# Performance work log

Measured on AMD Instinct MI355X. Metric: run time of the kernel, lower is better.

The kernel has to match this reference:

```python
import jax, jax.numpy as jnp
import numpy as np

DIM = 1024
HEADS = 16
DIM_HEAD = 64
INNER = HEADS * DIM_HEAD
EPS = 1e-6


def elu_feature_map(t):
    # F.elu(x) + 1
    return jnp.where(t > 0, t + 1.0, jnp.exp(t))


def setup_inputs() -> dict:
    key = jax.random.key(0)
    k1, k2, k3, k4 = jax.random.split(key, 4)
    B, N = 4, 8192
    x = jax.random.normal(k1, (B, N, DIM), dtype=jnp.float32)
    s_in = 1.0 / np.sqrt(DIM)
    s_out = 1.0 / np.sqrt(INNER)
    Wqkv = jax.random.uniform(k2, (DIM, 3 * INNER), dtype=jnp.float32, minval=-s_in, maxval=s_in)
    Wout = jax.random.uniform(k3, (INNER, DIM), dtype=jnp.float32, minval=-s_out, maxval=s_out)
    bout = jax.random.uniform(k4, (DIM,), dtype=jnp.float32, minval=-s_out, maxval=s_out)
    return {"x": x, "Wqkv": Wqkv, "Wout": Wout, "bout": bout}


def reference(x, Wqkv, Wout, bout):
    B, N, D = x.shape
    qkv = x @ Wqkv  # [B,N,3*INNER]
    q, k, v = jnp.split(qkv, 3, axis=-1)
    # b n (h d) -> b h n d
    resh = lambda t: t.reshape(B, N, HEADS, DIM_HEAD).transpose(0, 2, 1, 3)
    q, k, v = resh(q), resh(k), resh(v)
    q = elu_feature_map(q)
    k = elu_feature_map(k)
    kv = jnp.einsum('bhnd,bhnf->bhdf', k, v)          # [B,H,d,d]
    k_sum = k.sum(axis=-2)                             # [B,H,d]
    qkv_out = jnp.einsum('bhnd,bhdf->bhnf', q, kv)    # [B,H,N,d]
    q_k_sum = jnp.einsum('bhnd,bhd->bhn', q, k_sum)   # [B,H,N]
    out = qkv_out / (q_k_sum[..., None] + EPS)
    out = out.transpose(0, 2, 1, 3).reshape(B, N, INNER)  # b h n d -> b n (h d)
    return out @ Wout + bout
```

## Files before the change

### kernel.cpp

```cpp
#include <hip/hip_runtime.h>
#include <hip/hip_bf16.h>
#include <math.h>


typedef unsigned short ushort_t;
typedef __attribute__((ext_vector_type(8))) short s8v;
typedef __attribute__((ext_vector_type(4))) float f32x4;

#define MFMA(a,b,c) __builtin_amdgcn_mfma_f32_16x16x32_bf16((a),(b),(c),0,0,0)

typedef __attribute__((address_space(3))) unsigned int as3_u32;
typedef __attribute__((address_space(1))) const unsigned int as1_u32c;

__device__ __forceinline__ void g2l16(const void* g, void* l) {
    __builtin_amdgcn_global_load_lds((as1_u32c*)g, (as3_u32*)l, 16, 0, 0);
}

__device__ __forceinline__ float bf2f(ushort_t u) {
    union { float f; unsigned v; } x; x.v = ((unsigned)u) << 16; return x.f;
}
__device__ __forceinline__ ushort_t f2bf(float f) {
    union { float f; unsigned v; } x; x.f = f;
    unsigned r = x.v + 0x7fffu + ((x.v >> 16) & 1u);
    return (ushort_t)(r >> 16);
}
__device__ __forceinline__ float elu1(float t) { return t > 0.0f ? t + 1.0f : expf(t); }

__global__ void k_cast(const float* __restrict__ in, ushort_t* __restrict__ out, int n8) {
    int i = blockIdx.x * blockDim.x + threadIdx.x;
    if (i >= n8) return;
    const float4* p = (const float4*)in;
    float4 a = p[(size_t)i * 2], b = p[(size_t)i * 2 + 1];
    uint4 o;
    o.x = (unsigned)f2bf(a.x) | ((unsigned)f2bf(a.y) << 16);
    o.y = (unsigned)f2bf(a.z) | ((unsigned)f2bf(a.w) << 16);
    o.z = (unsigned)f2bf(b.x) | ((unsigned)f2bf(b.y) << 16);
    o.w = (unsigned)f2bf(b.z) | ((unsigned)f2bf(b.w) << 16);
    *(uint4*)(out + (size_t)i * 8) = o;
}

__global__ __launch_bounds__(256) void k_transpose(const float* __restrict__ W,
                                                   ushort_t* __restrict__ WT, int K, int N) {
    __shared__ float s[32][33];
    const int t = threadIdx.x;
    const int k0 = blockIdx.x * 32, n0 = blockIdx.y * 32;
    const int kr = t >> 3, n4 = (t & 7) * 4;
    float4 v = *(const float4*)(W + (size_t)(k0 + kr) * N + n0 + n4);
    s[kr][n4 + 0] = v.x; s[kr][n4 + 1] = v.y; s[kr][n4 + 2] = v.z; s[kr][n4 + 3] = v.w;
    __syncthreads();
    const int nr = kr, k4 = n4;
    unsigned lo = (unsigned)f2bf(s[k4 + 0][nr]) | ((unsigned)f2bf(s[k4 + 1][nr]) << 16);
    unsigned hi = (unsigned)f2bf(s[k4 + 2][nr]) | ((unsigned)f2bf(s[k4 + 3][nr]) << 16);
    *(uint2*)(WT + (size_t)(n0 + nr) * K + k0 + k4) = make_uint2(lo, hi);
}

template<int MODE>
__global__ __launch_bounds__(512, 2) void k_gemm(
    const ushort_t* __restrict__ A, const ushort_t* __restrict__ B,
    ushort_t* __restrict__ obf, const float* __restrict__ bout, float* __restrict__ of)
{
    constexpr int ASZ  = 256 * 64;
    constexpr int BUFS = 2 * ASZ;
    constexpr int NBN  = (MODE == 0) ? 12 : 4;
    constexpr int CH   = (128 * NBN) / 8;
    __shared__ ushort_t lds[2 * BUFS];

    const int t = threadIdx.x, l = t & 63, w = t >> 6;
    const int wr = w >> 2, wc = w & 3;
    const int orig = blockIdx.x;
    const int wg   = (orig & 7) * CH + (orig >> 3);
    const size_t m0 = (size_t)(wg / NBN) * 256;
    const size_t n0 = (size_t)(wg % NBN) * 256;

    f32x4 acc[8][4];
    const f32x4 z = {0.f, 0.f, 0.f, 0.f};
#pragma unroll
    for (int i = 0; i < 8; i++)
#pragma unroll
        for (int j = 0; j < 4; j++) acc[i][j] = z;

    const int lr  = l >> 3;
    const int lco = ((l & 7) ^ lr) << 3;
    const ushort_t* gA = A + (m0 + (size_t)(32 * w) + lr) * 1024 + lco;
    const ushort_t* gB = B + (n0 + (size_t)(32 * w) + lr) * 1024 + lco;
    const int la15 = l & 15;
    const int exo  = (((l >> 4) ^ (l & 7)) << 3);

#pragma unroll
    for (int i = 0; i < 4; i++)
        g2l16(gA + (size_t)(8 * i) * 1024, &lds[(w * 4 + i) * 512]);
#pragma unroll
    for (int i = 0; i < 4; i++)
        g2l16(gB + (size_t)(8 * i) * 1024, &lds[ASZ + (w * 4 + i) * 512]);
    asm volatile("s_waitcnt vmcnt(0)" ::: "memory");
    __builtin_amdgcn_sched_barrier(0);
    __builtin_amdgcn_s_barrier();
    __builtin_amdgcn_sched_barrier(0);

    for (int T = 0; T < 16; ++T) {
        const int base  = (T & 1) * BUFS;
        const int nbase = BUFS - base;

        if (T < 15) {
            const size_t k1 = (size_t)(T + 1) * 64;
#pragma unroll
            for (int i = 0; i < 4; i++)
                g2l16(gA + (size_t)(8 * i) * 1024 + k1, &lds[nbase + (w * 4 + i) * 512]);
#pragma unroll
            for (int i = 0; i < 4; i++)
                g2l16(gB + (size_t)(8 * i) * 1024 + k1, &lds[nbase + ASZ + (w * 4 + i) * 512]);
        }

        s8v af[8], bf[4];
#pragma unroll
        for (int nf = 0; nf < 4; nf++)
            bf[nf] = *(const s8v*)&lds[base + ASZ + (wc * 64 + nf * 16 + la15) * 64 + exo];
#pragma unroll
        for (int mf = 0; mf < 8; mf++)
            af[mf] = *(const s8v*)&lds[base + (wr * 128 + mf * 16 + la15) * 64 + exo];
        __builtin_amdgcn_s_setprio(1);
#pragma unroll
        for (int mf = 0; mf < 8; mf++)
#pragma unroll
            for (int nf = 0; nf < 4; nf++)
                acc[mf][nf] = MFMA(af[mf], bf[nf], acc[mf][nf]);
        __builtin_amdgcn_s_setprio(0);
#pragma unroll
        for (int nf = 0; nf < 4; nf++)
            bf[nf] = *(const s8v*)&lds[base + ASZ + (wc * 64 + nf * 16 + la15) * 64 + (32 ^ exo)];
#pragma unroll
        for (int mf = 0; mf < 8; mf++)
            af[mf] = *(const s8v*)&lds[base + (wr * 128 + mf * 16 + la15) * 64 + (32 ^ exo)];
        __builtin_amdgcn_s_setprio(1);
#pragma unroll
        for (int mf = 0; mf < 8; mf++)
#pragma unroll
            for (int nf = 0; nf < 4; nf++)
                acc[mf][nf] = MFMA(af[mf], bf[nf], acc[mf][nf]);
        __builtin_amdgcn_s_setprio(0);

        if (T < 15) {
            __builtin_amdgcn_sched_barrier(0);
            asm volatile("s_waitcnt vmcnt(0)" ::: "memory");
            __builtin_amdgcn_sched_barrier(0);
            __builtin_amdgcn_s_barrier();
            __builtin_amdgcn_sched_barrier(0);
        }
    }

    const int r4 = (l >> 4) * 4;
    if (MODE == 0) {
#pragma unroll
        for (int mf = 0; mf < 8; mf++)
#pragma unroll
            for (int nf = 0; nf < 4; nf++) {
                const size_t colb = n0 + wc * 64 + nf * 16;
                const bool feat = colb < 2048;
#pragma unroll
                for (int r = 0; r < 4; r++) {
                    const size_t row = m0 + wr * 128 + mf * 16 + r4 + r;
                    float v = acc[mf][nf][r];
                    obf[row * 3072 + colb + la15] = f2bf(feat ? elu1(v) : v);
                }
            }
    } else {
#pragma unroll
        for (int mf = 0; mf < 8; mf++)
#pragma unroll
            for (int nf = 0; nf < 4; nf++) {
                const size_t col = n0 + wc * 64 + nf * 16 + la15;
                const float bo = bout[col];
#pragma unroll
                for (int r = 0; r < 4; r++) {
                    const size_t row = m0 + wr * 128 + mf * 16 + r4 + r;
                    of[row * 1024 + col] = acc[mf][nf][r] + bo;
                }
            }
    }
}

#define KST 136
__global__ __launch_bounds__(256) void k_kv(
    const ushort_t* __restrict__ qkv, float* __restrict__ kv, float* __restrict__ ksum)
{
    __shared__ ushort_t kT[64 * KST];
    __shared__ ushort_t vT[64 * KST];
    __shared__ float ksl[64];
    const int t = threadIdx.x, l = t & 63, w = t >> 6;
    const int wr = w >> 1, wc = w & 1;
    const int h = blockIdx.x;
    const int b = blockIdx.z;
    const ushort_t* qkvb = qkv + (size_t)b * 8192 * 3072;
    float* kvh = kv + ((size_t)b * 16 + h) * 4096;
    float* ksh = ksum + (size_t)b * 1024 + h * 64;
    const int n00 = blockIdx.y * 512;
    const f32x4 z = {0.f, 0.f, 0.f, 0.f};
    f32x4 acc[2][2] = {{z, z}, {z, z}};
    float ksloc[4] = {0.f, 0.f, 0.f, 0.f};
    const int sd0 = (t & 15) * 4;
    const int tg  = t >> 4;
    if (t < 64) ksl[t] = 0.f;

    for (int c = 0; c < 4; c++) {
        __syncthreads();
        const int n0 = n00 + c * 128;
#pragma unroll
        for (int jj = 0; jj < 2; jj++) {
            const int nb = tg * 8 + jj * 4;
            ushort4 kw[4], vw[4];
#pragma unroll
            for (int j = 0; j < 4; j++) {
                const ushort_t* kp = qkvb + (size_t)(n0 + nb + j) * 3072 + 1024 + h * 64 + sd0;
                kw[j] = *(const ushort4*)kp;
                vw[j] = *(const ushort4*)(kp + 1024);
            }
#pragma unroll
            for (int j = 0; j < 4; j++) {
                ksloc[0] += bf2f(kw[j].x); ksloc[1] += bf2f(kw[j].y);
                ksloc[2] += bf2f(kw[j].z); ksloc[3] += bf2f(kw[j].w);
            }
            *(ushort4*)&kT[(sd0 + 0) * KST + nb] = make_ushort4(kw[0].x, kw[1].x, kw[2].x, kw[3].x);
            *(ushort4*)&kT[(sd0 + 1) * KST + nb] = make_ushort4(kw[0].y, kw[1].y, kw[2].y, kw[3].y);
            *(ushort4*)&kT[(sd0 + 2) * KST + nb] = make_ushort4(kw[0].z, kw[1].z, kw[2].z, kw[3].z);
            *(ushort4*)&kT[(sd0 + 3) * KST + nb] = make_ushort4(kw[0].w, kw[1].w, kw[2].w, kw[3].w);
            *(ushort4*)&vT[(sd0 + 0) * KST + nb] = make_ushort4(vw[0].x, vw[1].x, vw[2].x, vw[3].x);
            *(ushort4*)&vT[(sd0 + 1) * KST + nb] = make_ushort4(vw[0].y, vw[1].y, vw[2].y, vw[3].y);
            *(ushort4*)&vT[(sd0 + 2) * KST + nb] = make_ushort4(vw[0].z, vw[1].z, vw[2].z, vw[3].z);
            *(ushort4*)&vT[(sd0 + 3) * KST + nb] = make_ushort4(vw[0].w, vw[1].w, vw[2].w, vw[3].w);
        }
        __syncthreads();
#pragma unroll
        for (int kb = 0; kb < 128; kb += 32) {
            s8v af[2], bfr[2];
#pragma unroll
            for (int ma = 0; ma < 2; ma++) {
                int d = wr * 32 + ma * 16 + (l & 15);
                af[ma] = *(const s8v*)&kT[d * KST + kb + (l >> 4) * 8];
            }
#pragma unroll
            for (int fb = 0; fb < 2; fb++) {
                int f = wc * 32 + fb * 16 + (l & 15);
                bfr[fb] = *(const s8v*)&vT[f * KST + kb + (l >> 4) * 8];
            }
#pragma unroll
            for (int ma = 0; ma < 2; ma++)
#pragma unroll
                for (int fb = 0; fb < 2; fb++)
                    acc[ma][fb] = MFMA(af[ma], bfr[fb], acc[ma][fb]);
        }
    }
    atomicAdd(&ksl[sd0 + 0], ksloc[0]); atomicAdd(&ksl[sd0 + 1], ksloc[1]);
    atomicAdd(&ksl[sd0 + 2], ksloc[2]); atomicAdd(&ksl[sd0 + 3], ksloc[3]);
    __syncthreads();
    if (t < 64) atomicAdd(&ksh[t], ksl[t]);
#pragma unroll
    for (int ma = 0; ma < 2; ma++)
#pragma unroll
        for (int fb = 0; fb < 2; fb++)
#pragma unroll
            for (int r = 0; r < 4; r++) {
                int d = wr * 32 + ma * 16 + (l >> 4) * 4 + r;
                int f = wc * 32 + fb * 16 + (l & 15);
                atomicAdd(&kvh[f * 64 + d], acc[ma][fb][r]);
            }
}

#define AST 72
#define OST 520
__global__ __launch_bounds__(256) void k_apply(
    const ushort_t* __restrict__ qkv, const float* __restrict__ kv,
    const float* __restrict__ ksum, ushort_t* __restrict__ attn)
{
    __shared__ ushort_t kvb[64 * AST];
    __shared__ ushort_t obuf[32 * OST];
    const int t = threadIdx.x, l = t & 63, w = t >> 6;
    const int la15 = l & 15;
    const int row0 = blockIdx.x * 32;
    const int b = row0 >> 13;
    const f32x4 z = {0.f, 0.f, 0.f, 0.f};

    for (int hh = 0; hh < 8; hh++) {
        const int h = blockIdx.y * 8 + hh;
        const float* kvh = kv + ((size_t)b * 16 + h) * 4096;
        const float* ksh = ksum + (size_t)b * 1024 + h * 64;
        __syncthreads();
        {
            const int f = t >> 2, d0 = (t & 3) * 16;
            const float* src = kvh + f * 64 + d0;
            s8v v0, v1;
#pragma unroll
            for (int j = 0; j < 8; j++) {
                v0[j] = (short)f2bf(src[j]);
                v1[j] = (short)f2bf(src[j + 8]);
            }
            *(s8v*)&kvb[f * AST + d0]     = v0;
            *(s8v*)&kvb[f * AST + d0 + 8] = v1;
        }
        __syncthreads();
        float ksv[16];
        {
            const float* kp = ksh + (l >> 4) * 8;
            *(float4*)&ksv[0]  = *(const float4*)(kp);
            *(float4*)&ksv[4]  = *(const float4*)(kp + 4);
            *(float4*)&ksv[8]  = *(const float4*)(kp + 32);
            *(float4*)&ksv[12] = *(const float4*)(kp + 36);
        }
        f32x4 acc[2] = {z, z};
        float pd[2] = {0.f, 0.f};
#pragma unroll
        for (int ks = 0; ks < 2; ks++) {
            const int f = w * 16 + la15;
            s8v bfr = *(const s8v*)&kvb[f * AST + ks * 32 + (l >> 4) * 8];
#pragma unroll
            for (int ma = 0; ma < 2; ma++) {
                int row = row0 + ma * 16 + la15;
                s8v afr = *(const s8v*)(qkv + (size_t)row * 3072 + h * 64 + ks * 32 + (l >> 4) * 8);
#pragma unroll
                for (int j = 0; j < 8; j++)
                    pd[ma] += bf2f((ushort_t)afr[j]) * ksv[ks * 8 + j];
                acc[ma] = MFMA(afr, bfr, acc[ma]);
            }
        }
#pragma unroll
        for (int ma = 0; ma < 2; ma++) {
            pd[ma] += __shfl_xor(pd[ma], 16, 64);
            pd[ma] += __shfl_xor(pd[ma], 32, 64);
        }
#pragma unroll
        for (int ma = 0; ma < 2; ma++)
#pragma unroll
            for (int r = 0; r < 4; r++) {
                int lrow = (l >> 4) * 4 + r;
                float dot = __shfl(pd[ma], lrow, 64);
                float dv = 1.f / (dot + 1e-6f);
                int orow = ma * 16 + lrow;
                int ocol = hh * 64 + w * 16 + la15;
                obuf[orow * OST + ocol] = f2bf(acc[ma][r] * dv);
            }
    }
    __syncthreads();
    {
        const int row = t >> 3;
        const int c0  = (t & 7) * 8;
        ushort_t* dst = attn + (size_t)(row0 + row) * 1024 + blockIdx.y * 512;
#pragma unroll
        for (int i = 0; i < 8; i++) {
            const int col = c0 + i * 64;
            *(uint4*)(dst + col) = *(const uint4*)&obuf[row * OST + col];
        }
    }
}

extern "C" void kernel_launch(void* const* d_in, const int* in_sizes, int n_in,
                              void* d_out, int out_size, void* d_ws, size_t ws_size,
                              hipStream_t stream) {
    const float* x    = (const float*)d_in[0];
    const float* Wqkv = (const float*)d_in[1];
    const float* Wout = (const float*)d_in[2];
    const float* bout = (const float*)d_in[3];
    float* out = (float*)d_out;
    char* ws = (char*)d_ws;

    ushort_t* WqkvT = (ushort_t*)(ws + 0);
    ushort_t* WoutT = (ushort_t*)(ws + 6291456);
    float*    kv    = (float*)(ws + 8388608);
    float*    ksum  = (float*)(ws + 12582912);
    ushort_t* xb    = (ushort_t*)(ws + 12599296);
    ushort_t* qkv   = (ushort_t*)(ws + 79708160);
    ushort_t* attn  = (ushort_t*)(ws + 281034752);

    k_transpose<<<dim3(32, 96), 256, 0, stream>>>(Wqkv, WqkvT, 1024, 3072);
    k_transpose<<<dim3(32, 32), 256, 0, stream>>>(Wout, WoutT, 1024, 1024);
    hipMemsetAsync(kv, 0, 4194304 + 16384, stream);
    k_cast<<<16384, 256, 0, stream>>>(x, xb, 4194304);

    k_gemm<0><<<1536, 512, 0, stream>>>(xb, WqkvT, qkv, nullptr, nullptr);
    k_kv<<<dim3(16, 16, 4), 256, 0, stream>>>(qkv, kv, ksum);
    k_apply<<<dim3(1024, 2), 256, 0, stream>>>(qkv, kv, ksum, attn);
    k_gemm<1><<<512, 512, 0, stream>>>(attn, WoutT, nullptr, bout, out);
}
```

Before: 505.6 us.

## Halve GEMM K-tile to 32 and raise occupancy to four blocks per CU

Shrinks the per-stage K tile from 64 to 32, which halves LDS use per block, and doubles the loop count to 32 iterations with a matching swizzle for the narrower rows. Launch bounds change to 4 blocks of 512 threads per SM, and A fragments are loaded one at a time instead of all eight together, to cut register pressure. The aim is more resident waves to hide latency. In exchange there are twice as many barriers and waitcnt syncs per K sweep, and the tighter register budget may cause spills with the 128-float accumulator.

```diff
diff --git a/kernel.cpp b/kernel.cpp
--- a/kernel.cpp
+++ b/kernel.cpp
@@ -55,11 +55,11 @@
 }
 
 template<int MODE>
-__global__ __launch_bounds__(512, 2) void k_gemm(
+__global__ __launch_bounds__(512, 4) void k_gemm(
     const ushort_t* __restrict__ A, const ushort_t* __restrict__ B,
     ushort_t* __restrict__ obf, const float* __restrict__ bout, float* __restrict__ of)
 {
-    constexpr int ASZ  = 256 * 64;
+    constexpr int ASZ  = 256 * 32;
     constexpr int BUFS = 2 * ASZ;
     constexpr int NBN  = (MODE == 0) ? 12 : 4;
     constexpr int CH   = (128 * NBN) / 8;
@@ -79,67 +79,50 @@
 #pragma unroll
         for (int j = 0; j < 4; j++) acc[i][j] = z;
 
-    const int lr  = l >> 3;
-    const int lco = ((l & 7) ^ lr) << 3;
-    const ushort_t* gA = A + (m0 + (size_t)(32 * w) + lr) * 1024 + lco;
-    const ushort_t* gB = B + (n0 + (size_t)(32 * w) + lr) * 1024 + lco;
+    const int swz = (((l & 3) ^ ((l >> 2) & 3)) << 3);
+    const ushort_t* gA = A + (m0 + (size_t)(32 * w) + (l >> 2)) * 1024 + swz;
+    const ushort_t* gB = B + (n0 + (size_t)(32 * w) + (l >> 2)) * 1024 + swz;
+    const int dA = (32 * w) * 32;
+
     const int la15 = l & 15;
-    const int exo  = (((l >> 4) ^ (l & 7)) << 3);
-
-#pragma unroll
-    for (int i = 0; i < 4; i++)
-        g2l16(gA + (size_t)(8 * i) * 1024, &lds[(w * 4 + i) * 512]);
-#pragma unroll
-    for (int i = 0; i < 4; i++)
-        g2l16(gB + (size_t)(8 * i) * 1024, &lds[ASZ + (w * 4 + i) * 512]);
+    const int exo  = (((l >> 4) ^ (la15 & 3)) << 3);
+
+    g2l16(gA,              &lds[dA]);
+    g2l16(gA + 16 * 1024,  &lds[dA + 16 * 32]);
+    g2l16(gB,              &lds[ASZ + dA]);
+    g2l16(gB + 16 * 1024,  &lds[ASZ + dA + 16 * 32]);
     asm volatile("s_waitcnt vmcnt(0)" ::: "memory");
     __builtin_amdgcn_sched_barrier(0);
     __builtin_amdgcn_s_barrier();
     __builtin_amdgcn_sched_barrier(0);
 
-    for (int T = 0; T < 16; ++T) {
+    for (int T = 0; T < 32; ++T) {
         const int base  = (T & 1) * BUFS;
         const int nbase = BUFS - base;
 
-        if (T < 15) {
-            const size_t k1 = (size_t)(T + 1) * 64;
-#pragma unroll
-            for (int i = 0; i < 4; i++)
-                g2l16(gA + (size_t)(8 * i) * 1024 + k1, &lds[nbase + (w * 4 + i) * 512]);
-#pragma unroll
-            for (int i = 0; i < 4; i++)
-                g2l16(gB + (size_t)(8 * i) * 1024 + k1, &lds[nbase + ASZ + (w * 4 + i) * 512]);
-        }
-
-        s8v af[8], bf[4];
+        if (T < 31) {
+            const size_t k1 = (size_t)(T + 1) * 32;
+            g2l16(gA + k1,             &lds[nbase + dA]);
+            g2l16(gA + 16 * 1024 + k1, &lds[nbase + dA + 16 * 32]);
+            g2l16(gB + k1,             &lds[nbase + ASZ + dA]);
+            g2l16(gB + 16 * 1024 + k1, &lds[nbase + ASZ + dA + 16 * 32]);
+        }
+
+        s8v bf[4];
 #pragma unroll
         for (int nf = 0; nf < 4; nf++)
-            bf[nf] = *(const s8v*)&lds[base + ASZ + (wc * 64 + nf * 16 + la15) * 64 + exo];
-#pragma unroll
-        for (int mf = 0; mf < 8; mf++)
-            af[mf] = *(const s8v*)&lds[base + (wr * 128 + mf * 16 + la15) * 64 + exo];
-        __builtin_amdgcn_s_setprio(1);
-#pragma unroll
-        for (int mf = 0; mf < 8; mf++)
+            bf[nf] = *(const s8v*)&lds[base + ASZ + (wc * 64 + nf * 16 + la15) * 32 + exo];
+#pragma unroll
+        for (int mf = 0; mf < 8; mf++) {
+            s8v af = *(const s8v*)&lds[base + (wr * 128 + mf * 16 + la15) * 32 + exo];
+            __builtin_amdgcn_s_setprio(1);
 #pragma unroll
             for (int nf = 0; nf < 4; nf++)
-                acc[mf][nf] = MFMA(af[mf], bf[nf], acc[mf][nf]);
-        __builtin_amdgcn_s_setprio(0);
-#pragma unroll
-        for (int nf = 0; nf < 4; nf++)
-            bf[nf] = *(const s8v*)&lds[base + ASZ + (wc * 64 + nf * 16 + la15) * 64 + (32 ^ exo)];
-#pragma unroll
-        for (int mf = 0; mf < 8; mf++)
-            af[mf] = *(const s8v*)&lds[base + (wr * 128 + mf * 16 + la15) * 64 + (32 ^ exo)];
-        __builtin_amdgcn_s_setprio(1);
-#pragma unroll
-        for (int mf = 0; mf < 8; mf++)
-#pragma unroll
-            for (int nf = 0; nf < 4; nf++)
-                acc[mf][nf] = MFMA(af[mf], bf[nf], acc[mf][nf]);
-        __builtin_amdgcn_s_setprio(0);
-
-        if (T < 15) {
+                acc[mf][nf] = MFMA(af, bf[nf], acc[mf][nf]);
+            __builtin_amdgcn_s_setprio(0);
+        }
+
+        if (T < 31) {
             __builtin_amdgcn_sched_barrier(0);
             asm volatile("s_waitcnt vmcnt(0)" ::: "memory");
             __builtin_amdgcn_sched_barrier(0);
```

Measured after the change: 1.663 ms. 3.29x slower.
